# Kernel tuning notes

Hardware: AMD Instinct MI355X
Metric: run time of the kernel (lower is better)

Reference implementation:

```python
import jax, jax.numpy as jnp
import numpy as np

N = 50000        # nodes
E = 1500000      # edges
D = 128          # hidden_dim
L = 3            # layers_mp (t = 0..L-1)
RBAR = 1         # cfg.rbar -> delay = max(k - RBAR, 0)
EPS = 0.0        # GIN epsilon (not trainable)


def setup_inputs() -> dict:
    key = jax.random.key(0)
    ks = jax.random.split(key, 6)
    x = jax.random.normal(ks[0], (N, D), dtype=jnp.float32)
    edge_index = jax.random.randint(ks[1], (2, E), 0, N)          # [2, E] src/dst
    edge_attr = jax.random.randint(ks[2], (E,), 0, L)             # relation id k-1 in {0..L-1}
    # per-layer mlp_s: Linear(D, D) + ReLU
    Ws_s = jax.random.normal(ks[3], (L, D, D), dtype=jnp.float32) / np.float32(np.sqrt(D))
    bs_s = jnp.zeros((L, D), dtype=jnp.float32)
    # per-layer, per-relation mlp_k[k-1]: Linear(D, D) + ReLU (layer t uses k = 1..t+1)
    Ws_k = jax.random.normal(ks[4], (L, L, D, D), dtype=jnp.float32) / np.float32(np.sqrt(D))
    bs_k = jnp.zeros((L, L, D), dtype=jnp.float32)
    return dict(x=x, Ws_s=Ws_s, bs_s=bs_s, Ws_k=Ws_k, bs_k=bs_k,
                edge_index=edge_index, edge_attr=edge_attr)


def reference(x, Ws_s, bs_s, Ws_k, bs_k, edge_index, edge_attr):
    src, dst = edge_index[0], edge_index[1]
    n = x.shape[0]
    xs = []
    for t in range(L):
        xs.append(x)
        out = None
        for k in range(1, t + 2):
            delay = max(k - RBAR, 0)
            h_src = xs[t - delay]                       # delayed history for relation k
            # edge-type-grouped scatter-add: mask edges of relation k, gather, segment-sum
            mask = (edge_attr == (k - 1))
            msg = jnp.where(mask[:, None], h_src[src], jnp.float32(0.0))   # [E, D]
            agg = jax.ops.segment_sum(msg, dst, num_segments=n)            # [N, D]
            h = jax.nn.relu(agg @ Ws_k[t, k - 1] + bs_k[t, k - 1])         # mlp_k[k-1]
            out = h if out is None else out + h
        # self term: (1 + eps) * mlp_s(x); nn_post is identity (empty Sequential)
        out = out + (1.0 + EPS) * jax.nn.relu(x @ Ws_s[t] + bs_s[t])
        # outer loop: ReLU, dropout(p=0, eval), residual
        x = xs[-1] + jax.nn.relu(out)
    return x
```

## Files before the change

### kernel.cpp

```cpp
#include <hip/hip_runtime.h>

#define NN 50000
#define NE 1500000
#define DD 128
#define NRANGE ((NN + 255) / 256)
#define NBUCK (3 * NRANGE)
#define BINB 512
#define CHUNK ((NE + BINB - 1) / BINB)
#define NH2 (NBUCK * BINB)
#define GCONV ((NN * DD / 4 + 255) / 256)

typedef __attribute__((ext_vector_type(8))) short short8;
typedef __attribute__((ext_vector_type(4))) float f32x4;

__device__ __forceinline__ ushort f2b(float x) {
    uint u = __float_as_uint(x);
    u += 0x7FFFu + ((u >> 16) & 1u);
    return (ushort)(u >> 16);
}
__device__ __forceinline__ float b2f(ushort b) {
    return __uint_as_float(((uint)b) << 16);
}

__global__ __launch_bounds__(256) void scan_block(
    const int* __restrict__ cnt, int* __restrict__ ptr, int* __restrict__ part, int n)
{
    __shared__ int s[256];
    int i = blockIdx.x * 256 + threadIdx.x;
    int v = (i < n) ? cnt[i] : 0;
    s[threadIdx.x] = v;
    __syncthreads();
    #pragma unroll
    for (int off = 1; off < 256; off <<= 1) {
        int t = (threadIdx.x >= off) ? s[threadIdx.x - off] : 0;
        __syncthreads();
        s[threadIdx.x] += t;
        __syncthreads();
    }
    if (i < n) ptr[i] = s[threadIdx.x] - v;
    if (threadIdx.x == 255) part[blockIdx.x] = s[255];
}

__global__ void scan_partials(int* __restrict__ part, int nb)
{
    int lane = threadIdx.x;
    int run = 0;
    for (int base = 0; base < nb; base += 64) {
        int i = base + lane;
        int v = (i < nb) ? part[i] : 0;
        int x = v;
        #pragma unroll
        for (int off = 1; off < 64; off <<= 1) {
            int t = __shfl_up(x, off);
            if (lane >= off) x += t;
        }
        if (i < nb) part[i] = run + x - v;
        run += __shfl(x, 63);
    }
}

__global__ __launch_bounds__(256) void scan_add(
    int* __restrict__ ptr, const int* __restrict__ part, int n)
{
    int i = blockIdx.x * 256 + threadIdx.x;
    if (i >= n) return;
    ptr[i] += part[blockIdx.x];
}

__global__ __launch_bounds__(256) void prep_all(
    const int* __restrict__ dst, const int* __restrict__ attr, int* __restrict__ hist2,
    const float* __restrict__ x, ushort* __restrict__ xb,
    const float* __restrict__ Ws_s, const float* __restrict__ Ws_k, ushort* __restrict__ wt)
{
    __shared__ int lh[NBUCK];
    int b = blockIdx.x, tid = threadIdx.x;
    if (b < BINB) {
        for (int i = tid; i < NBUCK; i += 256) lh[i] = 0;
        __syncthreads();
        int lo = b * CHUNK, hi = lo + CHUNK; if (hi > NE) hi = NE;
        for (int e = lo + tid; e < hi; e += 256)
            atomicAdd(&lh[attr[e] * NRANGE + (dst[e] >> 8)], 1);
        __syncthreads();
        for (int i = tid; i < NBUCK; i += 256) hist2[i * BINB + b] = lh[i];
    } else if (b < BINB + GCONV) {
        int i = (b - BINB) * 256 + tid;
        if (i < NN * DD / 4) {
            float4 v = ((const float4*)x)[i];
            ushort4 o;
            o.x = f2b(v.x); o.y = f2b(v.y); o.z = f2b(v.z); o.w = f2b(v.w);
            ((ushort4*)xb)[i] = o;
        }
    } else {
        int i = (b - BINB - GCONV) * 256 + tid;
        if (i < 9 * 4096) {
            int m = i >> 12;
            int f = (i & 4095) * 4;
            int k = f >> 7, n = f & 127;
            const int tk[6] = {0, 3, 4, 6, 7, 8};
            const float* W = (m < 3) ? (Ws_s + (size_t)m * 16384)
                                     : (Ws_k + (size_t)tk[m - 3] * 16384);
            float4 v = *(const float4*)(W + (size_t)k * DD + n);
            ushort* o = wt + (size_t)m * 16384 + k;
            o[(size_t)(n + 0) * DD] = f2b(v.x);
            o[(size_t)(n + 1) * DD] = f2b(v.y);
            o[(size_t)(n + 2) * DD] = f2b(v.z);
            o[(size_t)(n + 3) * DD] = f2b(v.w);
        }
    }
}

__global__ __launch_bounds__(256) void binB(
    const int* __restrict__ src, const int* __restrict__ dst, const int* __restrict__ attr,
    const int* __restrict__ off2, uint* __restrict__ binned)
{
    __shared__ int lc[NBUCK];
    int tid = threadIdx.x, blk = blockIdx.x;
    for (int i = tid; i < NBUCK; i += 256) lc[i] = off2[i * BINB + blk];
    __syncthreads();
    int lo = blk * CHUNK, hi = lo + CHUNK; if (hi > NE) hi = NE;
    for (int e = lo + tid; e < hi; e += 256) {
        int d = dst[e];
        int b = attr[e] * NRANGE + (d >> 8);
        int pos = atomicAdd(&lc[b], 1);
        binned[pos] = (uint)src[e] | ((uint)(d & 255) << 16);
    }
}

__global__ __launch_bounds__(256) void bucket_finalize(
    const uint* __restrict__ binned, const int* __restrict__ off2,
    int* __restrict__ ptr, int* __restrict__ ssrc)
{
    __shared__ int lh[256];
    __shared__ int sc[256];
    __shared__ int cur[256];
    int b = blockIdx.x, tid = threadIdx.x;
    int rel = b / NRANGE, r0 = (b % NRANGE) << 8;
    int nloc = NN - r0; if (nloc > 256) nloc = 256;
    int lo = off2[b * BINB];
    int hi = (b + 1 < NBUCK) ? off2[(b + 1) * BINB] : NE;
    lh[tid] = 0;
    __syncthreads();
    for (int e = lo + tid; e < hi; e += 256)
        atomicAdd(&lh[(binned[e] >> 16) & 255], 1);
    __syncthreads();
    int v = lh[tid];
    sc[tid] = v;
    __syncthreads();
    #pragma unroll
    for (int off = 1; off < 256; off <<= 1) {
        int t = (tid >= off) ? sc[tid - off] : 0;
        __syncthreads();
        sc[tid] += t;
        __syncthreads();
    }
    int excl = lo + sc[tid] - v;
    if (tid < nloc) ptr[rel * NN + r0 + tid] = excl;
    cur[tid] = excl;
    if (b == NBUCK - 1 && tid == 0) ptr[3 * NN] = NE;
    __syncthreads();
    for (int e = lo + tid; e < hi; e += 256) {
        uint p = binned[e];
        int pos = atomicAdd(&cur[(p >> 16) & 255], 1);
        ssrc[pos] = (int)(p & 0xFFFFu);
    }
}

__global__ __launch_bounds__(256) void gather_multi(
    const ushort* __restrict__ h0, const ushort* __restrict__ h1,
    const ushort* __restrict__ h2,
    const int* __restrict__ ptr, const int* __restrict__ ssrc,
    ushort* __restrict__ a0, ushort* __restrict__ a1, ushort* __restrict__ a2)
{
    int rel = blockIdx.y;
    const ushort* h = (rel == 0) ? h0 : ((rel == 1) ? h1 : h2);
    ushort* agg     = (rel == 0) ? a0 : ((rel == 1) ? a1 : a2);

    int tid  = threadIdx.x;
    int half = (tid >> 5) & 1;
    int sub  = tid & 31;
    int n = blockIdx.x * 8 + ((tid >> 6) << 1) + half;
    if (n >= NN) return;
    const int* p = ptr + rel * NN + n;
    int s0 = p[0], s1 = p[1];
    float A0 = 0.f, A1 = 0.f, A2 = 0.f, A3 = 0.f;
    int e = s0;
    for (; e + 8 <= s1; e += 8) {
        int idx[8];
        #pragma unroll
        for (int j = 0; j < 8; ++j) idx[j] = ssrc[e + j];
        uint2 v[8];
        #pragma unroll
        for (int j = 0; j < 8; ++j)
            v[j] = ((const uint2*)(h + (size_t)idx[j] * DD))[sub];
        #pragma unroll
        for (int j = 0; j < 8; ++j) {
            A0 += b2f((ushort)(v[j].x & 0xFFFFu)); A1 += b2f((ushort)(v[j].x >> 16));
            A2 += b2f((ushort)(v[j].y & 0xFFFFu)); A3 += b2f((ushort)(v[j].y >> 16));
        }
    }
    if (e + 4 <= s1) {
        int i0 = ssrc[e], i1 = ssrc[e + 1], i2 = ssrc[e + 2], i3 = ssrc[e + 3];
        uint2 v0 = ((const uint2*)(h + (size_t)i0 * DD))[sub];
        uint2 v1 = ((const uint2*)(h + (size_t)i1 * DD))[sub];
        uint2 v2 = ((const uint2*)(h + (size_t)i2 * DD))[sub];
        uint2 v3 = ((const uint2*)(h + (size_t)i3 * DD))[sub];
        A0 += b2f((ushort)(v0.x & 0xFFFFu)); A1 += b2f((ushort)(v0.x >> 16));
        A2 += b2f((ushort)(v0.y & 0xFFFFu)); A3 += b2f((ushort)(v0.y >> 16));
        A0 += b2f((ushort)(v1.x & 0xFFFFu)); A1 += b2f((ushort)(v1.x >> 16));
        A2 += b2f((ushort)(v1.y & 0xFFFFu)); A3 += b2f((ushort)(v1.y >> 16));
        A0 += b2f((ushort)(v2.x & 0xFFFFu)); A1 += b2f((ushort)(v2.x >> 16));
        A2 += b2f((ushort)(v2.y & 0xFFFFu)); A3 += b2f((ushort)(v2.y >> 16));
        A0 += b2f((ushort)(v3.x & 0xFFFFu)); A1 += b2f((ushort)(v3.x >> 16));
        A2 += b2f((ushort)(v3.y & 0xFFFFu)); A3 += b2f((ushort)(v3.y >> 16));
        e += 4;
    }
    for (; e < s1; ++e) {
        int s = ssrc[e];
        uint2 v = ((const uint2*)(h + (size_t)s * DD))[sub];
        A0 += b2f((ushort)(v.x & 0xFFFFu)); A1 += b2f((ushort)(v.x >> 16));
        A2 += b2f((ushort)(v.y & 0xFFFFu)); A3 += b2f((ushort)(v.y >> 16));
    }
    uint2 o;
    o.x = (uint)f2b(A0) | ((uint)f2b(A1) << 16);
    o.y = (uint)f2b(A2) | ((uint)f2b(A3) << 16);
    ((uint2*)(agg + (size_t)n * DD))[sub] = o;
}

template<int NSRC, int WRITEF>
__global__ __launch_bounds__(256) void layer_mm(
    const ushort* __restrict__ s0, const ushort* __restrict__ s1,
    const ushort* __restrict__ s2, const ushort* __restrict__ s3,
    const ushort* __restrict__ w0, const ushort* __restrict__ w1,
    const ushort* __restrict__ w2, const ushort* __restrict__ w3,
    const float* __restrict__ b0, const float* __restrict__ b1,
    const float* __restrict__ b2, const float* __restrict__ b3,
    const ushort* __restrict__ xoldb, float* __restrict__ xnewf, ushort* __restrict__ xbnew)
{
    __shared__ ushort Atile[64 * 128];
    const int tid  = threadIdx.x;
    const int wave = tid >> 6, lane = tid & 63;
    const int row0 = blockIdx.x * 64;

    const ushort* srcs[4] = { s0, s1, s2, s3 };
    const ushort* wts[4]  = { w0, w1, w2, w3 };
    const float*  bss[4]  = { b0, b1, b2, b3 };

    float facc[4][2][4];
    #pragma unroll
    for (int rt = 0; rt < 4; ++rt)
        #pragma unroll
        for (int ct = 0; ct < 2; ++ct)
            #pragma unroll
            for (int q = 0; q < 4; ++q) facc[rt][ct][q] = 0.f;

    #pragma unroll
    for (int sidx = 0; sidx < NSRC; ++sidx) {
        const ushort* S = srcs[sidx];
        const ushort* W = wts[sidx];

        __syncthreads();
        for (int i = tid; i < 1024; i += 256) {
            int r = i >> 4, c = i & 15;
            int gr = row0 + r;
            uint4 v = make_uint4(0, 0, 0, 0);
            if (gr < NN) v = ((const uint4*)(S + (size_t)gr * DD))[c];
            int byte = ((r << 8) + (c << 4)) ^ ((r & 7) << 4);
            *((uint4*)((char*)Atile + byte)) = v;
        }
        short8 bfr[2][4];
        #pragma unroll
        for (int ct = 0; ct < 2; ++ct)
            #pragma unroll
            for (int ks = 0; ks < 4; ++ks) {
                int col = (wave << 5) + (ct << 4) + (lane & 15);
                int kb  = (ks << 5) + ((lane >> 4) << 3);
                bfr[ct][ks] = *(const short8*)(W + (size_t)col * DD + kb);
            }
        __syncthreads();

        f32x4 c[4][2];
        #pragma unroll
        for (int rt = 0; rt < 4; ++rt)
            #pragma unroll
            for (int ct = 0; ct < 2; ++ct) c[rt][ct] = (f32x4)(0.f);

        #pragma unroll
        for (int rt = 0; rt < 4; ++rt) {
            int row = (rt << 4) + (lane & 15);
            #pragma unroll
            for (int ks = 0; ks < 4; ++ks) {
                int byte = ((row << 8) + (ks << 6) + ((lane >> 4) << 4)) ^ ((row & 7) << 4);
                short8 a = *((const short8*)((const char*)Atile + byte));
                c[rt][0] = __builtin_amdgcn_mfma_f32_16x16x32_bf16(a, bfr[0][ks], c[rt][0], 0, 0, 0);
                c[rt][1] = __builtin_amdgcn_mfma_f32_16x16x32_bf16(a, bfr[1][ks], c[rt][1], 0, 0, 0);
            }
        }

        const float* B = bss[sidx];
        #pragma unroll
        for (int ct = 0; ct < 2; ++ct) {
            float bb = B[(wave << 5) + (ct << 4) + (lane & 15)];
            #pragma unroll
            for (int rt = 0; rt < 4; ++rt)
                #pragma unroll
                for (int q = 0; q < 4; ++q) {
                    float v = c[rt][ct][q] + bb;
                    facc[rt][ct][q] += v > 0.f ? v : 0.f;
                }
        }
    }

    #pragma unroll
    for (int rt = 0; rt < 4; ++rt)
        #pragma unroll
        for (int q = 0; q < 4; ++q) {
            int row = row0 + (rt << 4) + ((lane >> 4) << 2) + q;
            if (row >= NN) continue;
            #pragma unroll
            for (int ct = 0; ct < 2; ++ct) {
                int col = (wave << 5) + (ct << 4) + (lane & 15);
                size_t off = (size_t)row * DD + col;
                float v = facc[rt][ct][q] + b2f(xoldb[off]);
                xbnew[off] = f2b(v);
                if (WRITEF) xnewf[off] = v;
            }
        }
}

extern "C" void kernel_launch(void* const* d_in, const int* in_sizes, int n_in,
                              void* d_out, int out_size, void* d_ws, size_t ws_size,
                              hipStream_t stream) {
    const float* x0   = (const float*)d_in[0];
    const float* Ws_s = (const float*)d_in[1];
    const float* bs_s = (const float*)d_in[2];
    const float* Ws_k = (const float*)d_in[3];
    const float* bs_k = (const float*)d_in[4];
    const int*   src  = (const int*)d_in[5];
    const int*   dst  = src + NE;
    const int*   attr = (const int*)d_in[6];
    float* out = (float*)d_out;

    ushort* xb0  = (ushort*)d_ws;
    ushort* xb1  = xb0 + (size_t)NN * DD;
    ushort* xb2  = xb1 + (size_t)NN * DD;
    ushort* xb3  = xb2 + (size_t)NN * DD;
    ushort* P0   = xb3 + (size_t)NN * DD;
    ushort* P1   = P0 + (size_t)NN * DD;
    ushort* P2   = P1 + (size_t)NN * DD;
    ushort* wtb  = P2 + (size_t)NN * DD;
    int* ptr    = (int*)(wtb + 9 * 16384);
    int* part2  = ptr + 3 * NN + 1;
    int* ssrc   = part2 + 2048;
    uint* binned = (uint*)P0;
    int* hist2  = (int*)P1;
    int* off2   = hist2 + NH2;

    const int gGemm = (NN + 63) / 64;
    const int gGath = (NN + 7) / 8;
    const int NB2 = (NH2 + 255) / 256;

    auto wt = [&](int m) { return wtb + (size_t)m * 16384; };
    auto bk = [&](int t, int k) { return bs_k + ((size_t)t * 3 + k) * DD; };

    prep_all<<<BINB + GCONV + 144, 256, 0, stream>>>(
        dst, attr, hist2, x0, xb0, Ws_s, Ws_k, wtb);
    scan_block<<<NB2, 256, 0, stream>>>(hist2, off2, part2, NH2);
    scan_partials<<<1, 64, 0, stream>>>(part2, NB2);
    scan_add<<<NB2, 256, 0, stream>>>(off2, part2, NH2);
    binB<<<BINB, 256, 0, stream>>>(src, dst, attr, off2, binned);
    bucket_finalize<<<NBUCK, 256, 0, stream>>>(binned, off2, ptr, ssrc);

    gather_multi<<<dim3(gGath, 1), 256, 0, stream>>>(
        xb0, nullptr, nullptr, ptr, ssrc, P0, nullptr, nullptr);
    layer_mm<2, 0><<<gGemm, 256, 0, stream>>>(
        xb0, P0, nullptr, nullptr,
        wt(0), wt(3), nullptr, nullptr,
        bs_s, bk(0, 0), nullptr, nullptr,
        xb0, nullptr, xb1);

    gather_multi<<<dim3(gGath, 2), 256, 0, stream>>>(
        xb1, xb0, nullptr, ptr, ssrc, P0, P1, nullptr);
    layer_mm<3, 0><<<gGemm, 256, 0, stream>>>(
        xb1, P0, P1, nullptr,
        wt(1), wt(4), wt(5), nullptr,
        bs_s + DD, bk(1, 0), bk(1, 1), nullptr,
        xb1, nullptr, xb2);

    gather_multi<<<dim3(gGath, 3), 256, 0, stream>>>(
        xb2, xb1, xb0, ptr, ssrc, P0, P1, P2);
    layer_mm<4, 1><<<gGemm, 256, 0, stream>>>(
        xb2, P0, P1, P2,
        wt(2), wt(6), wt(7), wt(8),
        bs_s + 2 * DD, bk(2, 0), bk(2, 1), bk(2, 2),
        xb2, out, xb3);
}
```

Before: 267.2 us.

## Overlap delayed-history gathers with GEMM blocks in fused launches

Gathers whose source history is already known (relations 1 and 2 read older layer outputs) now run as extra blocks inside the preceding layer's GEMM kernel. This lets the bandwidth-bound gather work overlap the compute-bound matmul and cuts the number of gather passes on the critical path. Only the relation-0 gather stays as a separate launch between layers. The last layer also stops writing the unused bf16 copy of the output. The trade-off is that the fused kernels mix heterogeneous blocks and carry more buffers and parameters.

```diff
diff --git a/kernel.cpp b/kernel.cpp
--- a/kernel.cpp
+++ b/kernel.cpp
@@ -9,6 +9,8 @@
 #define CHUNK ((NE + BINB - 1) / BINB)
 #define NH2 (NBUCK * BINB)
 #define GCONV ((NN * DD / 4 + 255) / 256)
+#define GGEMM ((NN + 63) / 64)
+#define GGATH ((NN + 7) / 8)
 
 typedef __attribute__((ext_vector_type(8))) short short8;
 typedef __attribute__((ext_vector_type(4))) float f32x4;
@@ -165,20 +167,13 @@
     }
 }
 
-__global__ __launch_bounds__(256) void gather_multi(
-    const ushort* __restrict__ h0, const ushort* __restrict__ h1,
-    const ushort* __restrict__ h2,
-    const int* __restrict__ ptr, const int* __restrict__ ssrc,
-    ushort* __restrict__ a0, ushort* __restrict__ a1, ushort* __restrict__ a2)
-{
-    int rel = blockIdx.y;
-    const ushort* h = (rel == 0) ? h0 : ((rel == 1) ? h1 : h2);
-    ushort* agg     = (rel == 0) ? a0 : ((rel == 1) ? a1 : a2);
-
-    int tid  = threadIdx.x;
+__device__ __forceinline__ void gather_body(
+    const ushort* __restrict__ h, int rel, ushort* __restrict__ agg,
+    const int* __restrict__ ptr, const int* __restrict__ ssrc, int blk, int tid)
+{
     int half = (tid >> 5) & 1;
     int sub  = tid & 31;
-    int n = blockIdx.x * 8 + ((tid >> 6) << 1) + half;
+    int n = blk * 8 + ((tid >> 6) << 1) + half;
     if (n >= NN) return;
     const int* p = ptr + rel * NN + n;
     int s0 = p[0], s1 = p[1];
@@ -226,18 +221,38 @@
     ((uint2*)(agg + (size_t)n * DD))[sub] = o;
 }
 
-template<int NSRC, int WRITEF>
-__global__ __launch_bounds__(256) void layer_mm(
+__global__ __launch_bounds__(256) void gather_one(
+    const ushort* __restrict__ h, int rel,
+    const int* __restrict__ ptr, const int* __restrict__ ssrc,
+    ushort* __restrict__ agg)
+{
+    gather_body(h, rel, agg, ptr, ssrc, blockIdx.x, threadIdx.x);
+}
+
+template<int NSRC, int OUTMODE, int NG>
+__global__ __launch_bounds__(256) void mm_gather(
     const ushort* __restrict__ s0, const ushort* __restrict__ s1,
     const ushort* __restrict__ s2, const ushort* __restrict__ s3,
     const ushort* __restrict__ w0, const ushort* __restrict__ w1,
     const ushort* __restrict__ w2, const ushort* __restrict__ w3,
     const float* __restrict__ b0, const float* __restrict__ b1,
     const float* __restrict__ b2, const float* __restrict__ b3,
-    const ushort* __restrict__ xoldb, float* __restrict__ xnewf, ushort* __restrict__ xbnew)
+    const ushort* __restrict__ xoldb, float* __restrict__ xnewf, ushort* __restrict__ xbnew,
+    const ushort* __restrict__ g0tab, int g0rel, ushort* __restrict__ g0out,
+    const ushort* __restrict__ g1tab, int g1rel, ushort* __restrict__ g1out,
+    const int* __restrict__ ptr, const int* __restrict__ ssrc)
 {
     __shared__ ushort Atile[64 * 128];
-    const int tid  = threadIdx.x;
+    const int tid = threadIdx.x;
+
+    if (NG > 0 && blockIdx.x >= GGEMM) {
+        int g = blockIdx.x - GGEMM;
+        int which = (NG > 1) ? (g / GGATH) : 0;
+        gather_body(which ? g1tab : g0tab, which ? g1rel : g0rel,
+                    which ? g1out : g0out, ptr, ssrc, g % GGATH, tid);
+        return;
+    }
+
     const int wave = tid >> 6, lane = tid & 63;
     const int row0 = blockIdx.x * 64;
 
@@ -321,8 +336,8 @@
                 int col = (wave << 5) + (ct << 4) + (lane & 15);
                 size_t off = (size_t)row * DD + col;
                 float v = facc[rt][ct][q] + b2f(xoldb[off]);
-                xbnew[off] = f2b(v);
-                if (WRITEF) xnewf[off] = v;
+                if (OUTMODE == 0) xbnew[off] = f2b(v);
+                else              xnewf[off] = v;
             }
         }
 }
@@ -343,20 +358,18 @@
     ushort* xb0  = (ushort*)d_ws;
     ushort* xb1  = xb0 + (size_t)NN * DD;
     ushort* xb2  = xb1 + (size_t)NN * DD;
-    ushort* xb3  = xb2 + (size_t)NN * DD;
-    ushort* P0   = xb3 + (size_t)NN * DD;
-    ushort* P1   = P0 + (size_t)NN * DD;
-    ushort* P2   = P1 + (size_t)NN * DD;
-    ushort* wtb  = P2 + (size_t)NN * DD;
+    ushort* PA   = xb2 + (size_t)NN * DD;
+    ushort* PB   = PA + (size_t)NN * DD;
+    ushort* PC   = PB + (size_t)NN * DD;
+    ushort* PD   = PC + (size_t)NN * DD;
+    ushort* wtb  = PD + (size_t)NN * DD;
     int* ptr    = (int*)(wtb + 9 * 16384);
     int* part2  = ptr + 3 * NN + 1;
     int* ssrc   = part2 + 2048;
-    uint* binned = (uint*)P0;
-    int* hist2  = (int*)P1;
+    uint* binned = (uint*)PA;
+    int* hist2  = (int*)PB;
     int* off2   = hist2 + NH2;
 
-    const int gGemm = (NN + 63) / 64;
-    const int gGath = (NN + 7) / 8;
     const int NB2 = (NH2 + 255) / 256;
 
     auto wt = [&](int m) { return wtb + (size_t)m * 16384; };
@@ -370,27 +383,36 @@
     binB<<<BINB, 256, 0, stream>>>(src, dst, attr, off2, binned);
     bucket_finalize<<<NBUCK, 256, 0, stream>>>(binned, off2, ptr, ssrc);
 
-    gather_multi<<<dim3(gGath, 1), 256, 0, stream>>>(
-        xb0, nullptr, nullptr, ptr, ssrc, P0, nullptr, nullptr);
-    layer_mm<2, 0><<<gGemm, 256, 0, stream>>>(
-        xb0, P0, nullptr, nullptr,
+    gather_one<<<GGATH, 256, 0, stream>>>(xb0, 0, ptr, ssrc, PA);
+
+    mm_gather<2, 0, 2><<<GGEMM + 2 * GGATH, 256, 0, stream>>>(
+        xb0, PA, nullptr, nullptr,
         wt(0), wt(3), nullptr, nullptr,
         bs_s, bk(0, 0), nullptr, nullptr,
-        xb0, nullptr, xb1);
-
-    gather_multi<<<dim3(gGath, 2), 256, 0, stream>>>(
-        xb1, xb0, nullptr, ptr, ssrc, P0, P1, nullptr);
-    layer_mm<3, 0><<<gGemm, 256, 0, stream>>>(
-        xb1, P0, P1, nullptr,
+        xb0, nullptr, xb1,
+        xb0, 1, PB,
+        xb0, 2, PC,
+        ptr, ssrc);
+
+    gather_one<<<GGATH, 256, 0, stream>>>(xb1, 0, ptr, ssrc, PD);
+
+    mm_gather<3, 0, 1><<<GGEMM + GGATH, 256, 0, stream>>>(
+        xb1, PD, PB, nullptr,
         wt(1), wt(4), wt(5), nullptr,
         bs_s + DD, bk(1, 0), bk(1, 1), nullptr,
-        xb1, nullptr, xb2);
-
-    gather_multi<<<dim3(gGath, 3), 256, 0, stream>>>(
-        xb2, xb1, xb0, ptr, ssrc, P0, P1, P2);
-    layer_mm<4, 1><<<gGemm, 256, 0, stream>>>(
-        xb2, P0, P1, P2,
+        xb1, nullptr, xb2,
+        xb1, 1, PA,
+        nullptr, 0, nullptr,
+        ptr, ssrc);
+
+    gather_one<<<GGATH, 256, 0, stream>>>(xb2, 0, ptr, ssrc, PD);
+
+    mm_gather<4, 1, 0><<<GGEMM, 256, 0, stream>>>(
+        xb2, PD, PA, PC,
         wt(2), wt(6), wt(7), wt(8),
         bs_s + 2 * DD, bk(2, 0), bk(2, 1), bk(2, 2),
-        xb2, out, xb3);
-}
+        xb2, out, nullptr,
+        nullptr, 0, nullptr,
+        nullptr, 0, nullptr,
+        ptr, ssrc);
+}
```

Result: slower. 288.5 us (+8.0%).
